# Optimization experiments

Measured on AMD Instinct MI355X. Metric: run time of the kernel, lower is better.

The kernel has to match this reference:

```python
import jax, jax.numpy as jnp
import numpy as np

B, S, D = 32, 256, 768
H = 12
HD = D // H           # 64
MLP = 4 * D           # 3072
EPS = 1e-5


def layernorm(x, g, b):
    mu = jnp.mean(x, axis=-1, keepdims=True)
    var = jnp.mean((x - mu) ** 2, axis=-1, keepdims=True)
    return (x - mu) * jax.lax.rsqrt(var + EPS) * g + b


def setup_inputs() -> dict:
    key = jax.random.key(0)
    ks = jax.random.split(key, 16)
    s_head = 1.0 / np.sqrt(HD)
    s_d = 1.0 / np.sqrt(D)
    s_mlp = 1.0 / np.sqrt(MLP)
    return {
        "x": jax.random.normal(ks[0], (B, S, D), dtype=jnp.float32),
        "g1": jnp.ones((D,), jnp.float32),
        "beta1": jnp.zeros((D,), jnp.float32),
        # per-head linear weights, torch Linear layout [out, in] stacked over heads
        "Wq": jax.random.uniform(ks[1], (H, HD, HD), jnp.float32, -s_head, s_head),
        "bq": jax.random.uniform(ks[2], (H, HD), jnp.float32, -s_head, s_head),
        "Wk": jax.random.uniform(ks[3], (H, HD, HD), jnp.float32, -s_head, s_head),
        "bk": jax.random.uniform(ks[4], (H, HD), jnp.float32, -s_head, s_head),
        "Wv": jax.random.uniform(ks[5], (H, HD, HD), jnp.float32, -s_head, s_head),
        "bv": jax.random.uniform(ks[6], (H, HD), jnp.float32, -s_head, s_head),
        "g2": jnp.ones((D,), jnp.float32),
        "beta2": jnp.zeros((D,), jnp.float32),
        "W1": jax.random.uniform(ks[7], (MLP, D), jnp.float32, -s_d, s_d),
        "bm1": jax.random.uniform(ks[8], (MLP,), jnp.float32, -s_d, s_d),
        "W2": jax.random.uniform(ks[9], (D, MLP), jnp.float32, -s_mlp, s_mlp),
        "bm2": jax.random.uniform(ks[10], (D,), jnp.float32, -s_mlp, s_mlp),
    }


def reference(x, g1, beta1, Wq, bq, Wk, bk, Wv, bv, g2, beta2, W1, bm1, W2, bm2):
    # --- MHA on norm1(x), fused over batch and heads ---
    h = layernorm(x, g1, beta1)                      # [B,S,D]
    hh = h.reshape(B, S, H, HD)                      # head split matches slicing in Mymha
    # q_e = sum_d hh_d * W[e,d]  (torch Linear: y = x @ W.T + b)
    q = jnp.einsum('bshd,hed->bshe', hh, Wq) + bq
    k = jnp.einsum('bshd,hed->bshe', hh, Wk) + bk
    v = jnp.einsum('bshd,hed->bshe', hh, Wv) + bv
    scores = jnp.einsum('bshe,bthe->bhst', q, k) / np.sqrt(HD)
    attn = jax.nn.softmax(scores, axis=-1)           # [B,H,S,S]
    ctx = jnp.einsum('bhst,bthe->bshe', attn, v).reshape(B, S, D)
    out = ctx + x
    # --- MLP on norm2(out) ---
    h2 = layernorm(out, g2, beta2)
    m = jax.nn.gelu(h2 @ W1.T + bm1, approximate=False)  # torch nn.GELU is exact erf
    out = m @ W2.T + bm2 + out
    return out
```

## Files before the change

kernel.cpp:

```cpp
#include <hip/hip_runtime.h>
#include <hip/hip_bf16.h>
#include <math.h>


static constexpr int Bn = 32, Sn = 256, Dn = 768, Hn = 12, HDn = 64, MLPn = 3072;
static constexpr int NT = Bn * Sn;

typedef unsigned short ushort_t;
typedef unsigned int u32;
typedef __attribute__((ext_vector_type(8))) short short8;
typedef __attribute__((ext_vector_type(4))) float f32x4;

__device__ __forceinline__ float bf2f(ushort_t u) { return __uint_as_float(((u32)u) << 16); }
__device__ __forceinline__ ushort_t f2bf(float f) {
  u32 u = __float_as_uint(f);
  u += 0x7fffu + ((u >> 16) & 1u);
  return (ushort_t)(u >> 16);
}

__device__ __forceinline__ void async_cp16(const ushort_t* g, ushort_t* l) {
  __builtin_amdgcn_global_load_lds(
      (const __attribute__((address_space(1))) u32*)g,
      (__attribute__((address_space(3))) u32*)l, 16, 0, 0);
}

__global__ __launch_bounds__(256) void k_prep(
    const float* __restrict__ Wq, const float* __restrict__ Wk,
    const float* __restrict__ Wv, const float* __restrict__ bq,
    const float* __restrict__ bk, const float* __restrict__ bv,
    const float* __restrict__ W1, const float* __restrict__ W2,
    const float* __restrict__ x, const float* __restrict__ g1,
    const float* __restrict__ be1,
    ushort_t* __restrict__ Wc, float* __restrict__ bc,
    ushort_t* __restrict__ W1b, ushort_t* __restrict__ W2b,
    ushort_t* __restrict__ hb)
{
  __shared__ float red[8];
  const int bx = blockIdx.x;
  const int tid = threadIdx.x;
  if (bx < 576) {
    int i = bx * 256 + tid;
    int h = i / 12288, rem = i - h * 12288;
    int mat = rem / 4096, w = rem - mat * 4096;
    const float* src = (mat == 0) ? Wq : ((mat == 1) ? Wk : Wv);
    Wc[i] = f2bf(src[h * 4096 + w]);
    if (i < Hn * 192) {
      int h2 = i / 192, r2 = i - h2 * 192;
      int m2 = r2 / 64, e2 = r2 - m2 * 64;
      const float* bs = (m2 == 0) ? bq : ((m2 == 1) ? bk : bv);
      bc[i] = bs[h2 * 64 + e2];
    }
  } else if (bx < 5184) {
    int j = bx - 576;
    const float* src = (j < 2304) ? W1 : W2;
    ushort_t* dst = (j < 2304) ? W1b : W2b;
    int i = (j % 2304) * 256 + tid;
    float4 v = ((const float4*)src)[i];
    ushort4 o;
    o.x = f2bf(v.x); o.y = f2bf(v.y); o.z = f2bf(v.z); o.w = f2bf(v.w);
    ((ushort4*)dst)[i] = o;
  } else {
    const int t = bx - 5184;
    float xv[3];
#pragma unroll
    for (int i = 0; i < 3; i++) xv[i] = x[(size_t)t * Dn + tid + i * 256];
    float s = xv[0] + xv[1] + xv[2];
#pragma unroll
    for (int off = 32; off > 0; off >>= 1) s += __shfl_down(s, off, 64);
    if ((tid & 63) == 0) red[tid >> 6] = s;
    __syncthreads();
    float mean = (red[0] + red[1] + red[2] + red[3]) * (1.0f / 768.0f);
    float d0 = xv[0] - mean, d1 = xv[1] - mean, d2 = xv[2] - mean;
    float s2 = d0 * d0 + d1 * d1 + d2 * d2;
#pragma unroll
    for (int off = 32; off > 0; off >>= 1) s2 += __shfl_down(s2, off, 64);
    if ((tid & 63) == 0) red[4 + (tid >> 6)] = s2;
    __syncthreads();
    float rstd = rsqrtf((red[4] + red[5] + red[6] + red[7]) * (1.0f / 768.0f) + 1e-5f);
#pragma unroll
    for (int i = 0; i < 3; i++) {
      int d = tid + i * 256;
      hb[(size_t)t * Dn + d] = f2bf((xv[i] - mean) * rstd * g1[d] + be1[d]);
    }
  }
}

__global__ __launch_bounds__(256) void k_qkv(
    const ushort_t* __restrict__ hb,
    const ushort_t* __restrict__ Wc,
    const float* __restrict__ bc,
    ushort_t* __restrict__ qo, ushort_t* __restrict__ ko, ushort_t* __restrict__ vt)
{
  __shared__ __align__(16) ushort_t As[128 * 72];
  __shared__ __align__(16) ushort_t Ws[192 * 72];
  const int blk = blockIdx.x;
  const int half = blk & 1;
  const int bh = blk >> 1;
  const int b_ = bh / Hn, h_ = bh - b_ * Hn;
  const int tid = threadIdx.x;
  const int t0 = b_ * Sn + half * 128;

  {
    int row = tid >> 1, seg = (tid & 1) * 32;
    const uint4* g = (const uint4*)(hb + (size_t)(t0 + row) * Dn + h_ * 64 + seg);
    uint4* s = (uint4*)(As + row * 72 + seg);
    s[0] = g[0]; s[1] = g[1]; s[2] = g[2]; s[3] = g[3];
  }
  {
    int rr = tid >> 2, seg = (tid & 3) * 16;
    const ushort_t* gw = Wc + h_ * 12288;
#pragma unroll
    for (int p = 0; p < 3; p++) {
      int R = p * 64 + rr;
      const uint4* g = (const uint4*)(gw + R * 64 + seg);
      uint4* s = (uint4*)(Ws + R * 72 + seg);
      s[0] = g[0]; s[1] = g[1];
    }
  }
  __syncthreads();

  const int wave = tid >> 6, lane = tid & 63;
  const int wm = (wave >> 1) * 64, wn = (wave & 1) * 96;
  const int lrow = lane & 15, quad = lane >> 4;

  f32x4 acc[4][6];
#pragma unroll
  for (int mi = 0; mi < 4; mi++)
#pragma unroll
    for (int ni = 0; ni < 6; ni++) acc[mi][ni] = (f32x4){0.f, 0.f, 0.f, 0.f};

#pragma unroll
  for (int kk = 0; kk < 2; kk++) {
    short8 af[4], wf[6];
#pragma unroll
    for (int mi = 0; mi < 4; mi++)
      af[mi] = *(const short8*)(As + (wm + mi * 16 + lrow) * 72 + kk * 32 + quad * 8);
#pragma unroll
    for (int ni = 0; ni < 6; ni++)
      wf[ni] = *(const short8*)(Ws + (wn + ni * 16 + lrow) * 72 + kk * 32 + quad * 8);
#pragma unroll
    for (int mi = 0; mi < 4; mi++)
#pragma unroll
      for (int ni = 0; ni < 6; ni++)
        acc[mi][ni] = __builtin_amdgcn_mfma_f32_16x16x32_bf16(af[mi], wf[ni], acc[mi][ni], 0, 0, 0);
  }

#pragma unroll
  for (int ni = 0; ni < 6; ni++) {
    int c = wn + ni * 16 + lrow;
    int mat = c >> 6, e = c & 63;
    float bb = bc[h_ * 192 + c];
    if (mat < 2) {
      ushort_t* dst = (mat == 0) ? qo : ko;
      size_t base = (((size_t)bh) * Sn + half * 128 + wm) * HDn + e;
#pragma unroll
      for (int mi = 0; mi < 4; mi++) {
#pragma unroll
        for (int r = 0; r < 4; r++) {
          int lr = mi * 16 + quad * 4 + r;
          dst[base + (size_t)lr * HDn] = f2bf(acc[mi][ni][r] + bb);
        }
      }
    } else {
      size_t rowb = ((size_t)bh * 64 + e) * Sn + half * 128 + wm + quad * 4;
#pragma unroll
      for (int mi = 0; mi < 4; mi++) {
        ushort4 pk;
        pk.x = f2bf(acc[mi][ni][0] + bb);
        pk.y = f2bf(acc[mi][ni][1] + bb);
        pk.z = f2bf(acc[mi][ni][2] + bb);
        pk.w = f2bf(acc[mi][ni][3] + bb);
        *(ushort4*)(vt + rowb + mi * 16) = pk;
      }
    }
  }
}

__global__ __launch_bounds__(256) void k_attn(
    const ushort_t* __restrict__ q,
    const ushort_t* __restrict__ kg_,
    const ushort_t* __restrict__ vt,
    const float* __restrict__ x,
    float* __restrict__ out1)
{
  __shared__ __align__(16) ushort_t Ks[64 * 72];
  __shared__ __align__(16) ushort_t Vts[64 * 264];
  __shared__ __align__(16) ushort_t Pw[4][16 * 72];
  const int blk = blockIdx.x;
  const int qtr = blk & 3, bh = blk >> 2;
  const int b_ = bh / Hn, h_ = bh - b_ * Hn;
  const int tid = threadIdx.x, wave = tid >> 6, lane = tid & 63;
  const int lr16 = lane & 15, quad = lane >> 4;
  const int s0 = qtr * 64 + wave * 16;

  {
    int r = tid >> 2, cseg = (tid & 3) * 64;
    const uint4* g = (const uint4*)(vt + ((size_t)bh * 64 + r) * Sn + cseg);
    uint4* s = (uint4*)(Vts + r * 264 + cseg);
#pragma unroll
    for (int i = 0; i < 8; i++) s[i] = g[i];
  }

  short8 qf[2];
  {
    const ushort_t* qg = q + ((size_t)bh * Sn + s0 + lr16) * HDn + quad * 8;
    qf[0] = *(const short8*)(qg);
    qf[1] = *(const short8*)(qg + 32);
  }

  f32x4 of[4];
#pragma unroll
  for (int et = 0; et < 4; et++) of[et] = (f32x4){0.f, 0.f, 0.f, 0.f};
  float mrow[4] = {-3.0e38f, -3.0e38f, -3.0e38f, -3.0e38f};
  float lsum[4] = {0.f, 0.f, 0.f, 0.f};

  const ushort_t* kgb = kg_ + (size_t)bh * Sn * HDn;

  for (int c = 0; c < 4; c++) {
    if (c) __syncthreads();
    {
      int row = tid >> 2, seg = (tid & 3) * 16;
      const uint4* g = (const uint4*)(kgb + (size_t)(c * 64 + row) * HDn + seg);
      uint4* s = (uint4*)(Ks + row * 72 + seg);
      s[0] = g[0]; s[1] = g[1];
    }
    __syncthreads();

    f32x4 sc[4];
#pragma unroll
    for (int ni = 0; ni < 4; ni++) sc[ni] = (f32x4){0.f, 0.f, 0.f, 0.f};
#pragma unroll
    for (int kk = 0; kk < 2; kk++) {
#pragma unroll
      for (int ni = 0; ni < 4; ni++) {
        short8 kf = *(const short8*)(Ks + (ni * 16 + lr16) * 72 + kk * 32 + quad * 8);
        sc[ni] = __builtin_amdgcn_mfma_f32_16x16x32_bf16(qf[kk], kf, sc[ni], 0, 0, 0);
      }
    }

    float alpha[4];
#pragma unroll
    for (int r = 0; r < 4; r++) {
      float m_ = fmaxf(fmaxf(sc[0][r], sc[1][r]), fmaxf(sc[2][r], sc[3][r]));
#pragma unroll
      for (int msk = 8; msk >= 1; msk >>= 1) m_ = fmaxf(m_, __shfl_xor(m_, msk, 64));
      float mn = fmaxf(mrow[r], m_);
      alpha[r] = __expf((mrow[r] - mn) * 0.125f);
      mrow[r] = mn;
    }
#pragma unroll
    for (int ni = 0; ni < 4; ni++) {
#pragma unroll
      for (int r = 0; r < 4; r++) {
        float p = __expf((sc[ni][r] - mrow[r]) * 0.125f);
        sc[ni][r] = p;
        Pw[wave][(quad * 4 + r) * 72 + ni * 16 + lr16] = f2bf(p);
      }
    }
#pragma unroll
    for (int r = 0; r < 4; r++) {
      float s_ = (sc[0][r] + sc[1][r]) + (sc[2][r] + sc[3][r]);
#pragma unroll
      for (int msk = 8; msk >= 1; msk >>= 1) s_ += __shfl_xor(s_, msk, 64);
      lsum[r] = lsum[r] * alpha[r] + s_;
    }
#pragma unroll
    for (int et = 0; et < 4; et++)
#pragma unroll
      for (int r = 0; r < 4; r++) of[et][r] *= alpha[r];

    short8 pf0 = *(const short8*)(&Pw[wave][lr16 * 72 + quad * 8]);
    short8 pf1 = *(const short8*)(&Pw[wave][lr16 * 72 + 32 + quad * 8]);
#pragma unroll
    for (int et = 0; et < 4; et++) {
      short8 vf0 = *(const short8*)(Vts + (et * 16 + lr16) * 264 + c * 64 + quad * 8);
      short8 vf1 = *(const short8*)(Vts + (et * 16 + lr16) * 264 + c * 64 + 32 + quad * 8);
      of[et] = __builtin_amdgcn_mfma_f32_16x16x32_bf16(pf0, vf0, of[et], 0, 0, 0);
      of[et] = __builtin_amdgcn_mfma_f32_16x16x32_bf16(pf1, vf1, of[et], 0, 0, 0);
    }
  }

  const size_t obase = ((size_t)b_ * Sn + s0) * Dn + h_ * 64;
#pragma unroll
  for (int r = 0; r < 4; r++) {
    float rl = 1.0f / lsum[r];
    int row = quad * 4 + r;
#pragma unroll
    for (int et = 0; et < 4; et++) {
      size_t idx = obase + (size_t)row * Dn + et * 16 + lr16;
      out1[idx] = of[et][r] * rl + x[idx];
    }
  }
}

__global__ __launch_bounds__(256) void k_ln2(
    const float* __restrict__ in, const float* __restrict__ g2,
    const float* __restrict__ be2, ushort_t* __restrict__ h2)
{
  const int t = blockIdx.x, tid = threadIdx.x;
  __shared__ float red[8];
  float xv[3];
#pragma unroll
  for (int i = 0; i < 3; i++) xv[i] = in[(size_t)t * Dn + tid + i * 256];
  float s = xv[0] + xv[1] + xv[2];
#pragma unroll
  for (int off = 32; off > 0; off >>= 1) s += __shfl_down(s, off, 64);
  if ((tid & 63) == 0) red[tid >> 6] = s;
  __syncthreads();
  float mean = (red[0] + red[1] + red[2] + red[3]) * (1.0f / 768.0f);
  float d0 = xv[0] - mean, d1 = xv[1] - mean, d2 = xv[2] - mean;
  float s2 = d0 * d0 + d1 * d1 + d2 * d2;
#pragma unroll
  for (int off = 32; off > 0; off >>= 1) s2 += __shfl_down(s2, off, 64);
  if ((tid & 63) == 0) red[4 + (tid >> 6)] = s2;
  __syncthreads();
  float rstd = rsqrtf((red[4] + red[5] + red[6] + red[7]) * (1.0f / 768.0f) + 1e-5f);
#pragma unroll
  for (int i = 0; i < 3; i++) {
    int d = tid + i * 256;
    h2[(size_t)t * Dn + d] = f2bf((xv[i] - mean) * rstd * g2[d] + be2[d]);
  }
}

__global__ __launch_bounds__(512, 2) void k_gemm1(
    const ushort_t* __restrict__ A,
    const ushort_t* __restrict__ Bw,
    const float* __restrict__ bias,
    ushort_t* __restrict__ CoutB)
{
  constexpr int KD = Dn;
  constexpr int NTILES = 12;
  constexpr int BUFU = 28672;
  __shared__ __align__(16) ushort_t smem[57344];
  const int b = blockIdx.x;
  const int xcd = b & 7, slot = b >> 3;
  const int cc = slot % 16, rloc = slot / 16;
  const int m0 = (xcd * 4 + rloc) * 256, n0 = cc * 192;
  const int tid = threadIdx.x;
  const int wave = tid >> 6, lane = tid & 63;
  const int wm2 = (wave >> 2) * 128, wn2 = (wave & 3) * 48;
  const int lrow = lane & 15, quad = lane >> 4;
  const int key = lrow & 7;

  f32x4 acc[8][3];
#pragma unroll
  for (int mi = 0; mi < 8; mi++)
#pragma unroll
    for (int ni = 0; ni < 3; ni++) acc[mi][ni] = (f32x4){0.f, 0.f, 0.f, 0.f};

  auto stageA = [&](int t, int half) {
    if (t >= NTILES) return;
    const int k0 = t * 64;
    ushort_t* tb = smem + (t & 1) * BUFU + half * 8192;
#pragma unroll
    for (int j = 0; j < 2; ++j) {
      int q = j * 512 + tid;
      int row = q >> 3;
      int sc = (q & 7) ^ (row & 7);
      async_cp16(A + (size_t)(m0 + half * 128 + row) * KD + k0 + sc * 8, tb + q * 8);
    }
  };
  auto stageB = [&](int t) {
    if (t >= NTILES) return;
    const int k0 = t * 64;
    ushort_t* tb = smem + (t & 1) * BUFU + 16384;
#pragma unroll
    for (int j = 0; j < 3; ++j) {
      int q = j * 512 + tid;
      int row = q >> 3;
      int sc = (q & 7) ^ (row & 7);
      async_cp16(Bw + (size_t)(n0 + row) * KD + k0 + sc * 8, tb + q * 8);
    }
  };

  stageA(0, 0); stageA(0, 1); stageB(0);
  asm volatile("s_waitcnt vmcnt(0)" ::: "memory");
  __builtin_amdgcn_s_barrier();
  __builtin_amdgcn_sched_barrier(0);

  short8 af[4][2], af2[4][2], bf0[3], bf1[3];
  for (int t = 0; t < NTILES; ++t) {
    const ushort_t* Ab = smem + (t & 1) * BUFU;
    const ushort_t* Bb = Ab + 16384;

#pragma unroll
    for (int mi = 0; mi < 4; ++mi)
#pragma unroll
      for (int kk = 0; kk < 2; ++kk)
        af[mi][kk] = *(const short8*)(Ab + (wm2 + mi * 16 + lrow) * 64 + (((kk << 2) + quad) ^ key) * 8);
#pragma unroll
    for (int ni = 0; ni < 3; ++ni)
      bf0[ni] = *(const short8*)(Bb + (wn2 + ni * 16 + lrow) * 64 + ((quad ^ key) * 8));
    stageA(t + 1, 0);
    __builtin_amdgcn_s_barrier();
    asm volatile("s_waitcnt lgkmcnt(0)" ::: "memory");
    __builtin_amdgcn_sched_barrier(0);
    __builtin_amdgcn_s_setprio(1);
#pragma unroll
    for (int mi = 0; mi < 4; ++mi)
#pragma unroll
      for (int ni = 0; ni < 3; ++ni)
        acc[mi][ni] = __builtin_amdgcn_mfma_f32_16x16x32_bf16(af[mi][0], bf0[ni], acc[mi][ni], 0, 0, 0);
    __builtin_amdgcn_s_setprio(0);
    __builtin_amdgcn_s_barrier();
    __builtin_amdgcn_sched_barrier(0);

#pragma unroll
    for (int ni = 0; ni < 3; ++ni)
      bf1[ni] = *(const short8*)(Bb + (wn2 + ni * 16 + lrow) * 64 + (((4 + quad) ^ key) * 8));
#pragma unroll
    for (int mi = 0; mi < 4; ++mi)
#pragma unroll
      for (int kk = 0; kk < 2; ++kk)
        af2[mi][kk] = *(const short8*)(Ab + (wm2 + 64 + mi * 16 + lrow) * 64 + (((kk << 2) + quad) ^ key) * 8);
    stageA(t + 1, 1);
    __builtin_amdgcn_s_barrier();
    asm volatile("s_waitcnt lgkmcnt(0)" ::: "memory");
    __builtin_amdgcn_sched_barrier(0);
    __builtin_amdgcn_s_setprio(1);
#pragma unroll
    for (int mi = 0; mi < 4; ++mi)
#pragma unroll
      for (int ni = 0; ni < 3; ++ni)
        acc[mi][ni] = __builtin_amdgcn_mfma_f32_16x16x32_bf16(af[mi][1], bf1[ni], acc[mi][ni], 0, 0, 0);
    __builtin_amdgcn_s_setprio(0);
    __builtin_amdgcn_s_barrier();
    __builtin_amdgcn_sched_barrier(0);

    stageB(t + 1);
    __builtin_amdgcn_s_barrier();
    __builtin_amdgcn_sched_barrier(0);
    __builtin_amdgcn_s_setprio(1);
#pragma unroll
    for (int mi = 0; mi < 4; ++mi)
#pragma unroll
      for (int ni = 0; ni < 3; ++ni)
        acc[4 + mi][ni] = __builtin_amdgcn_mfma_f32_16x16x32_bf16(af2[mi][0], bf0[ni], acc[4 + mi][ni], 0, 0, 0);
    __builtin_amdgcn_s_setprio(0);
    __builtin_amdgcn_s_barrier();
    __builtin_amdgcn_sched_barrier(0);

    __builtin_amdgcn_s_setprio(1);
#pragma unroll
    for (int mi = 0; mi < 4; ++mi)
#pragma unroll
      for (int ni = 0; ni < 3; ++ni)
        acc[4 + mi][ni] = __builtin_amdgcn_mfma_f32_16x16x32_bf16(af2[mi][1], bf1[ni], acc[4 + mi][ni], 0, 0, 0);
    __builtin_amdgcn_s_setprio(0);
    asm volatile("s_waitcnt vmcnt(0)" ::: "memory");
    __builtin_amdgcn_s_barrier();
    __builtin_amdgcn_sched_barrier(0);
  }

  float bwv[3];
#pragma unroll
  for (int ni = 0; ni < 3; ++ni) bwv[ni] = bias[n0 + wn2 + ni * 16 + lrow];
  __syncthreads();
#pragma unroll
  for (int mi = 0; mi < 8; ++mi) {
#pragma unroll
    for (int ni = 0; ni < 3; ++ni) {
      int col = wn2 + ni * 16 + lrow;
#pragma unroll
      for (int r = 0; r < 4; ++r) {
        int row = wm2 + mi * 16 + quad * 4 + r;
        float vv = acc[mi][ni][r] + bwv[ni];
        float u = vv * (0.7978845608f + 0.0356774081f * vv * vv);
        float o = vv / (1.0f + __expf(-2.0f * u));
        smem[row * 200 + col] = f2bf(o);
      }
    }
  }
  __syncthreads();
#pragma unroll
  for (int i = 0; i < 12; ++i) {
    int idx = i * 512 + tid;
    int rr = idx / 24, ck = idx - rr * 24;
    const uint4 v = *(const uint4*)(smem + rr * 200 + ck * 8);
    *(uint4*)(CoutB + (size_t)(m0 + rr) * MLPn + n0 + ck * 8) = v;
  }
}

__global__ __launch_bounds__(512, 2) void k_gemm2(
    const ushort_t* __restrict__ A,
    const ushort_t* __restrict__ Bw,
    const float* __restrict__ bias,
    const float* __restrict__ res,
    float* __restrict__ out)
{
  constexpr int KD = MLPn;
  constexpr int N = Dn;
  constexpr int NTILES = 48;
  constexpr int BUFU = 20480;
  __shared__ __align__(16) ushort_t smem[61440];
  const int b = blockIdx.x;
  const int xcd = b & 7, slot = b >> 3;
  const int cc = slot & 3, rloc = slot >> 2;
  const int m0 = (xcd * 8 + rloc) * 128, n0 = cc * 192;
  const int tid = threadIdx.x;
  const int wave = tid >> 6, lane = tid & 63;
  const int wm2 = (wave >> 2) * 64, wn2 = (wave & 3) * 48;
  const int lrow = lane & 15, quad = lane >> 4;
  const int key = lrow & 7;

  f32x4 acc[4][3];
#pragma unroll
  for (int mi = 0; mi < 4; mi++)
#pragma unroll
    for (int ni = 0; ni < 3; ni++) acc[mi][ni] = (f32x4){0.f, 0.f, 0.f, 0.f};

  auto stageT = [&](int t) {
    if (t >= NTILES) return;
    const int k0 = t * 64;
    ushort_t* bufA = smem + (t % 3) * BUFU;
    ushort_t* bufB = bufA + 8192;
#pragma unroll
    for (int j = 0; j < 2; ++j) {
      int q = j * 512 + tid;
      int row = q >> 3;
      int sc = (q & 7) ^ (row & 7);
      async_cp16(A + (size_t)(m0 + row) * KD + k0 + sc * 8, bufA + q * 8);
    }
#pragma unroll
    for (int j = 0; j < 3; ++j) {
      int q = j * 512 + tid;
      int row = q >> 3;
      int sc = (q & 7) ^ (row & 7);
      async_cp16(Bw + (size_t)(n0 + row) * KD + k0 + sc * 8, bufB + q * 8);
    }
  };

  stageT(0); stageT(1);
  asm volatile("s_waitcnt vmcnt(5)" ::: "memory");
  __builtin_amdgcn_s_barrier();
  __builtin_amdgcn_sched_barrier(0);

  short8 af[4], bf[3];
  for (int t = 0; t < NTILES; ++t) {
    const ushort_t* Ab = smem + (t % 3) * BUFU;
    const ushort_t* Bb = Ab + 8192;

#pragma unroll
    for (int mi = 0; mi < 4; ++mi)
      af[mi] = *(const short8*)(Ab + (wm2 + mi * 16 + lrow) * 64 + ((quad ^ key) * 8));
#pragma unroll
    for (int ni = 0; ni < 3; ++ni)
      bf[ni] = *(const short8*)(Bb + (wn2 + ni * 16 + lrow) * 64 + ((quad ^ key) * 8));
    stageT(t + 2);
    asm volatile("s_waitcnt lgkmcnt(0)" ::: "memory");
    __builtin_amdgcn_sched_barrier(0);
    __builtin_amdgcn_s_setprio(1);
#pragma unroll
    for (int mi = 0; mi < 4; ++mi)
#pragma unroll
      for (int ni = 0; ni < 3; ++ni)
        acc[mi][ni] = __builtin_amdgcn_mfma_f32_16x16x32_bf16(af[mi], bf[ni], acc[mi][ni], 0, 0, 0);
    __builtin_amdgcn_s_setprio(0);
#pragma unroll
    for (int mi = 0; mi < 4; ++mi)
      af[mi] = *(const short8*)(Ab + (wm2 + mi * 16 + lrow) * 64 + (((4 + quad) ^ key) * 8));
#pragma unroll
    for (int ni = 0; ni < 3; ++ni)
      bf[ni] = *(const short8*)(Bb + (wn2 + ni * 16 + lrow) * 64 + (((4 + quad) ^ key) * 8));
    asm volatile("s_waitcnt lgkmcnt(0)" ::: "memory");
    __builtin_amdgcn_sched_barrier(0);
    __builtin_amdgcn_s_setprio(1);
#pragma unroll
    for (int mi = 0; mi < 4; ++mi)
#pragma unroll
      for (int ni = 0; ni < 3; ++ni)
        acc[mi][ni] = __builtin_amdgcn_mfma_f32_16x16x32_bf16(af[mi], bf[ni], acc[mi][ni], 0, 0, 0);
    __builtin_amdgcn_s_setprio(0);
    if (t < NTILES - 2) {
      asm volatile("s_waitcnt vmcnt(5)" ::: "memory");
    } else {
      asm volatile("s_waitcnt vmcnt(0)" ::: "memory");
    }
    __builtin_amdgcn_s_barrier();
    __builtin_amdgcn_sched_barrier(0);
  }

#pragma unroll
  for (int ni = 0; ni < 3; ++ni) {
    int col = n0 + wn2 + ni * 16 + lrow;
    float bc = bias[col];
#pragma unroll
    for (int mi = 0; mi < 4; ++mi) {
#pragma unroll
      for (int r = 0; r < 4; ++r) {
        int row = m0 + wm2 + mi * 16 + quad * 4 + r;
        size_t idx = (size_t)row * N + col;
        out[idx] = acc[mi][ni][r] + bc + res[idx];
      }
    }
  }
}

extern "C" void kernel_launch(void* const* d_in, const int* in_sizes, int n_in,
                              void* d_out, int out_size, void* d_ws, size_t ws_size,
                              hipStream_t stream) {
  (void)in_sizes; (void)n_in; (void)out_size; (void)ws_size;
  const float* x   = (const float*)d_in[0];
  const float* g1  = (const float*)d_in[1];
  const float* be1 = (const float*)d_in[2];
  const float* Wq  = (const float*)d_in[3];
  const float* bq  = (const float*)d_in[4];
  const float* Wk  = (const float*)d_in[5];
  const float* bk  = (const float*)d_in[6];
  const float* Wv  = (const float*)d_in[7];
  const float* bv  = (const float*)d_in[8];
  const float* g2  = (const float*)d_in[9];
  const float* be2 = (const float*)d_in[10];
  const float* W1  = (const float*)d_in[11];
  const float* bm1 = (const float*)d_in[12];
  const float* W2  = (const float*)d_in[13];
  const float* bm2 = (const float*)d_in[14];
  float* outp = (float*)d_out;

  char* ws = (char*)d_ws;
  float*    out1 = (float*)ws;
  ushort_t* hb   = (ushort_t*)ws;
  ushort_t* qb   = (ushort_t*)(ws + 25165824);
  ushort_t* kb   = (ushort_t*)(ws + 37748736);
  ushort_t* vtb  = (ushort_t*)(ws + 50331648);
  ushort_t* h2   = qb;
  ushort_t* mb   = (ushort_t*)(ws + 37748736);
  ushort_t* Wc   = (ushort_t*)(ws + 88080384);
  ushort_t* W1b  = (ushort_t*)(ws + 88375296);
  ushort_t* W2b  = (ushort_t*)(ws + 93093888);
  float*    bcb  = (float*)(ws + 97812480);

  k_prep<<<dim3(5184 + NT), dim3(256), 0, stream>>>(Wq, Wk, Wv, bq, bk, bv, W1, W2,
                                                    x, g1, be1, Wc, bcb, W1b, W2b, hb);
  k_qkv<<<dim3(Bn * Hn * 2), dim3(256), 0, stream>>>(hb, Wc, bcb, qb, kb, vtb);
  k_attn<<<dim3(Bn * Hn * 4), dim3(256), 0, stream>>>(qb, kb, vtb, x, out1);
  k_ln2<<<dim3(NT), dim3(256), 0, stream>>>(out1, g2, be2, h2);
  k_gemm1<<<dim3(512), dim3(512), 0, stream>>>(h2, W1b, bm1, mb);
  k_gemm2<<<dim3(256), dim3(512), 0, stream>>>(mb, W2b, bm2, out1, outp);
}
```

Before: 270.9 us.

## Fuse QKV projection and attention into one kernel keeping Q/K/V in LDS

Merges the per-head QKV projection and the attention kernel so that each block computes Q, K and V for one (batch, head) into XOR-swizzled shared memory and then runs attention directly from LDS. This removes the global round-trip of Q, K and V^T and one kernel launch. The input loads now use async global-to-LDS copies, and softmax switches from online to a single pass over all 256 keys. The cost is 152 KB of LDS per block, which allows only one block per CU, and a grid of 384 blocks, down from 768 and 1536 before, which lowers occupancy and parallelism.

```diff
diff --git a/kernel.cpp b/kernel.cpp
--- a/kernel.cpp
+++ b/kernel.cpp
@@ -85,210 +85,171 @@
   }
 }
 
-__global__ __launch_bounds__(256) void k_qkv(
+__global__ __launch_bounds__(256) void k_fused(
     const ushort_t* __restrict__ hb,
     const ushort_t* __restrict__ Wc,
     const float* __restrict__ bc,
-    ushort_t* __restrict__ qo, ushort_t* __restrict__ ko, ushort_t* __restrict__ vt)
-{
-  __shared__ __align__(16) ushort_t As[128 * 72];
-  __shared__ __align__(16) ushort_t Ws[192 * 72];
-  const int blk = blockIdx.x;
-  const int half = blk & 1;
-  const int bh = blk >> 1;
-  const int b_ = bh / Hn, h_ = bh - b_ * Hn;
-  const int tid = threadIdx.x;
-  const int t0 = b_ * Sn + half * 128;
-
-  {
-    int row = tid >> 1, seg = (tid & 1) * 32;
-    const uint4* g = (const uint4*)(hb + (size_t)(t0 + row) * Dn + h_ * 64 + seg);
-    uint4* s = (uint4*)(As + row * 72 + seg);
-    s[0] = g[0]; s[1] = g[1]; s[2] = g[2]; s[3] = g[3];
-  }
-  {
-    int rr = tid >> 2, seg = (tid & 3) * 16;
-    const ushort_t* gw = Wc + h_ * 12288;
-#pragma unroll
-    for (int p = 0; p < 3; p++) {
-      int R = p * 64 + rr;
-      const uint4* g = (const uint4*)(gw + R * 64 + seg);
-      uint4* s = (uint4*)(Ws + R * 72 + seg);
-      s[0] = g[0]; s[1] = g[1];
-    }
-  }
-  __syncthreads();
-
-  const int wave = tid >> 6, lane = tid & 63;
-  const int wm = (wave >> 1) * 64, wn = (wave & 1) * 96;
-  const int lrow = lane & 15, quad = lane >> 4;
-
-  f32x4 acc[4][6];
-#pragma unroll
-  for (int mi = 0; mi < 4; mi++)
-#pragma unroll
-    for (int ni = 0; ni < 6; ni++) acc[mi][ni] = (f32x4){0.f, 0.f, 0.f, 0.f};
-
-#pragma unroll
-  for (int kk = 0; kk < 2; kk++) {
-    short8 af[4], wf[6];
-#pragma unroll
-    for (int mi = 0; mi < 4; mi++)
-      af[mi] = *(const short8*)(As + (wm + mi * 16 + lrow) * 72 + kk * 32 + quad * 8);
-#pragma unroll
-    for (int ni = 0; ni < 6; ni++)
-      wf[ni] = *(const short8*)(Ws + (wn + ni * 16 + lrow) * 72 + kk * 32 + quad * 8);
-#pragma unroll
-    for (int mi = 0; mi < 4; mi++)
-#pragma unroll
-      for (int ni = 0; ni < 6; ni++)
-        acc[mi][ni] = __builtin_amdgcn_mfma_f32_16x16x32_bf16(af[mi], wf[ni], acc[mi][ni], 0, 0, 0);
-  }
-
-#pragma unroll
-  for (int ni = 0; ni < 6; ni++) {
-    int c = wn + ni * 16 + lrow;
-    int mat = c >> 6, e = c & 63;
-    float bb = bc[h_ * 192 + c];
-    if (mat < 2) {
-      ushort_t* dst = (mat == 0) ? qo : ko;
-      size_t base = (((size_t)bh) * Sn + half * 128 + wm) * HDn + e;
-#pragma unroll
-      for (int mi = 0; mi < 4; mi++) {
-#pragma unroll
-        for (int r = 0; r < 4; r++) {
-          int lr = mi * 16 + quad * 4 + r;
-          dst[base + (size_t)lr * HDn] = f2bf(acc[mi][ni][r] + bb);
-        }
-      }
-    } else {
-      size_t rowb = ((size_t)bh * 64 + e) * Sn + half * 128 + wm + quad * 4;
-#pragma unroll
-      for (int mi = 0; mi < 4; mi++) {
-        ushort4 pk;
-        pk.x = f2bf(acc[mi][ni][0] + bb);
-        pk.y = f2bf(acc[mi][ni][1] + bb);
-        pk.z = f2bf(acc[mi][ni][2] + bb);
-        pk.w = f2bf(acc[mi][ni][3] + bb);
-        *(ushort4*)(vt + rowb + mi * 16) = pk;
-      }
-    }
-  }
-}
-
-__global__ __launch_bounds__(256) void k_attn(
-    const ushort_t* __restrict__ q,
-    const ushort_t* __restrict__ kg_,
-    const ushort_t* __restrict__ vt,
     const float* __restrict__ x,
     float* __restrict__ out1)
 {
-  __shared__ __align__(16) ushort_t Ks[64 * 72];
-  __shared__ __align__(16) ushort_t Vts[64 * 264];
-  __shared__ __align__(16) ushort_t Pw[4][16 * 72];
-  const int blk = blockIdx.x;
-  const int qtr = blk & 3, bh = blk >> 2;
+  __shared__ __align__(16) ushort_t smem[77824];
+  ushort_t* Qs  = smem;
+  ushort_t* Ks  = smem + 16384;
+  ushort_t* Vts = smem + 32768;
+  ushort_t* As  = smem + 49152;
+  ushort_t* Ws  = smem + 65536;
+  ushort_t* Pw  = smem + 49152;
+
+  const int bh = blockIdx.x;
   const int b_ = bh / Hn, h_ = bh - b_ * Hn;
-  const int tid = threadIdx.x, wave = tid >> 6, lane = tid & 63;
-  const int lr16 = lane & 15, quad = lane >> 4;
-  const int s0 = qtr * 64 + wave * 16;
+  const int tid = threadIdx.x;
+  const int wave = tid >> 6, lane = tid & 63;
+  const int lrow = lane & 15, quad = lane >> 4;
+  const int key = lrow & 7;
+  const int t0 = b_ * Sn;
 
   {
-    int r = tid >> 2, cseg = (tid & 3) * 64;
-    const uint4* g = (const uint4*)(vt + ((size_t)bh * 64 + r) * Sn + cseg);
-    uint4* s = (uint4*)(Vts + r * 264 + cseg);
-#pragma unroll
-    for (int i = 0; i < 8; i++) s[i] = g[i];
-  }
-
-  short8 qf[2];
-  {
-    const ushort_t* qg = q + ((size_t)bh * Sn + s0 + lr16) * HDn + quad * 8;
-    qf[0] = *(const short8*)(qg);
-    qf[1] = *(const short8*)(qg + 32);
-  }
-
-  f32x4 of[4];
-#pragma unroll
-  for (int et = 0; et < 4; et++) of[et] = (f32x4){0.f, 0.f, 0.f, 0.f};
-  float mrow[4] = {-3.0e38f, -3.0e38f, -3.0e38f, -3.0e38f};
-  float lsum[4] = {0.f, 0.f, 0.f, 0.f};
-
-  const ushort_t* kgb = kg_ + (size_t)bh * Sn * HDn;
-
-  for (int c = 0; c < 4; c++) {
-    if (c) __syncthreads();
-    {
-      int row = tid >> 2, seg = (tid & 3) * 16;
-      const uint4* g = (const uint4*)(kgb + (size_t)(c * 64 + row) * HDn + seg);
-      uint4* s = (uint4*)(Ks + row * 72 + seg);
-      s[0] = g[0]; s[1] = g[1];
-    }
-    __syncthreads();
-
-    f32x4 sc[4];
-#pragma unroll
-    for (int ni = 0; ni < 4; ni++) sc[ni] = (f32x4){0.f, 0.f, 0.f, 0.f};
+    const ushort_t* ga = hb + (size_t)t0 * Dn + h_ * 64;
+#pragma unroll
+    for (int j = 0; j < 8; ++j) {
+      int q = j * 256 + tid;
+      int row = q >> 3;
+      int sc = (q & 7) ^ (row & 7);
+      async_cp16(ga + (size_t)row * Dn + sc * 8, As + q * 8);
+    }
+    const ushort_t* gw = Wc + h_ * 12288;
+#pragma unroll
+    for (int j = 0; j < 6; ++j) {
+      int q = j * 256 + tid;
+      int row = q >> 3;
+      int sc = (q & 7) ^ (row & 7);
+      async_cp16(gw + row * 64 + sc * 8, Ws + q * 8);
+    }
+  }
+  asm volatile("s_waitcnt vmcnt(0)" ::: "memory");
+  __syncthreads();
+
+  const int wm = (wave >> 1) * 64, wn = (wave & 1) * 96;
+  for (int half = 0; half < 2; ++half) {
+    f32x4 acc[4][6];
+#pragma unroll
+    for (int mi = 0; mi < 4; mi++)
+#pragma unroll
+      for (int ni = 0; ni < 6; ni++) acc[mi][ni] = (f32x4){0.f, 0.f, 0.f, 0.f};
+
 #pragma unroll
     for (int kk = 0; kk < 2; kk++) {
-#pragma unroll
-      for (int ni = 0; ni < 4; ni++) {
-        short8 kf = *(const short8*)(Ks + (ni * 16 + lr16) * 72 + kk * 32 + quad * 8);
+      short8 af[4], wf[6];
+#pragma unroll
+      for (int mi = 0; mi < 4; mi++)
+        af[mi] = *(const short8*)(As + (half * 128 + wm + mi * 16 + lrow) * 64 + ((((kk << 2) + quad)) ^ key) * 8);
+#pragma unroll
+      for (int ni = 0; ni < 6; ni++)
+        wf[ni] = *(const short8*)(Ws + (wn + ni * 16 + lrow) * 64 + ((((kk << 2) + quad)) ^ key) * 8);
+#pragma unroll
+      for (int mi = 0; mi < 4; mi++)
+#pragma unroll
+        for (int ni = 0; ni < 6; ni++)
+          acc[mi][ni] = __builtin_amdgcn_mfma_f32_16x16x32_bf16(af[mi], wf[ni], acc[mi][ni], 0, 0, 0);
+    }
+
+#pragma unroll
+    for (int ni = 0; ni < 6; ni++) {
+      int c = wn + ni * 16 + lrow;
+      int mat = c >> 6, e = c & 63;
+      float bb = bc[h_ * 192 + c];
+      if (mat < 2) {
+        ushort_t* dst = (mat == 0) ? Qs : Ks;
+#pragma unroll
+        for (int mi = 0; mi < 4; mi++) {
+#pragma unroll
+          for (int r = 0; r < 4; r++) {
+            int srow = half * 128 + wm + mi * 16 + quad * 4 + r;
+            dst[srow * 64 + (((e >> 3) ^ (srow & 7)) << 3) + (e & 7)] = f2bf(acc[mi][ni][r] + bb);
+          }
+        }
+      } else {
+#pragma unroll
+        for (int mi = 0; mi < 4; mi++) {
+          int c4 = half * 128 + wm + mi * 16 + quad * 4;
+          ushort4 pk;
+          pk.x = f2bf(acc[mi][ni][0] + bb);
+          pk.y = f2bf(acc[mi][ni][1] + bb);
+          pk.z = f2bf(acc[mi][ni][2] + bb);
+          pk.w = f2bf(acc[mi][ni][3] + bb);
+          int cq = c4 >> 3;
+          *(ushort4*)(Vts + e * 256 + ((cq ^ (e & 7)) << 3) + (c4 & 7)) = pk;
+        }
+      }
+    }
+  }
+  __syncthreads();
+
+  ushort_t* Pme = Pw + wave * 4224;
+  for (int p = 0; p < 4; ++p) {
+    const int s0 = wave * 64 + p * 16;
+    short8 qf[2];
+#pragma unroll
+    for (int kk = 0; kk < 2; kk++)
+      qf[kk] = *(const short8*)(Qs + (s0 + lrow) * 64 + ((((kk << 2) + quad)) ^ key) * 8);
+
+    f32x4 sc[16];
+#pragma unroll
+    for (int ni = 0; ni < 16; ni++) sc[ni] = (f32x4){0.f, 0.f, 0.f, 0.f};
+#pragma unroll
+    for (int kk = 0; kk < 2; kk++) {
+#pragma unroll
+      for (int ni = 0; ni < 16; ni++) {
+        short8 kf = *(const short8*)(Ks + (ni * 16 + lrow) * 64 + ((((kk << 2) + quad)) ^ key) * 8);
         sc[ni] = __builtin_amdgcn_mfma_f32_16x16x32_bf16(qf[kk], kf, sc[ni], 0, 0, 0);
       }
     }
 
-    float alpha[4];
+    float inv[4];
 #pragma unroll
     for (int r = 0; r < 4; r++) {
-      float m_ = fmaxf(fmaxf(sc[0][r], sc[1][r]), fmaxf(sc[2][r], sc[3][r]));
+      float m_ = sc[0][r];
+#pragma unroll
+      for (int ni = 1; ni < 16; ni++) m_ = fmaxf(m_, sc[ni][r]);
 #pragma unroll
       for (int msk = 8; msk >= 1; msk >>= 1) m_ = fmaxf(m_, __shfl_xor(m_, msk, 64));
-      float mn = fmaxf(mrow[r], m_);
-      alpha[r] = __expf((mrow[r] - mn) * 0.125f);
-      mrow[r] = mn;
-    }
-#pragma unroll
-    for (int ni = 0; ni < 4; ni++) {
-#pragma unroll
-      for (int r = 0; r < 4; r++) {
-        float p = __expf((sc[ni][r] - mrow[r]) * 0.125f);
-        sc[ni][r] = p;
-        Pw[wave][(quad * 4 + r) * 72 + ni * 16 + lr16] = f2bf(p);
-      }
-    }
+      float s_ = 0.f;
+#pragma unroll
+      for (int ni = 0; ni < 16; ni++) {
+        float pv = __expf((sc[ni][r] - m_) * 0.125f);
+        s_ += pv;
+        Pme[(quad * 4 + r) * 264 + ni * 16 + lrow] = f2bf(pv);
+      }
+#pragma unroll
+      for (int msk = 8; msk >= 1; msk >>= 1) s_ += __shfl_xor(s_, msk, 64);
+      inv[r] = 1.0f / s_;
+    }
+    asm volatile("s_waitcnt lgkmcnt(0)" ::: "memory");
+    __builtin_amdgcn_sched_barrier(0);
+
+    f32x4 of[4];
+#pragma unroll
+    for (int et = 0; et < 4; et++) of[et] = (f32x4){0.f, 0.f, 0.f, 0.f};
+#pragma unroll
+    for (int ks = 0; ks < 8; ks++) {
+      short8 pf = *(const short8*)(Pme + lrow * 264 + ks * 32 + quad * 8);
+#pragma unroll
+      for (int et = 0; et < 4; et++) {
+        short8 vf = *(const short8*)(Vts + (et * 16 + lrow) * 256 + ((((ks << 2) + quad)) ^ key) * 8);
+        of[et] = __builtin_amdgcn_mfma_f32_16x16x32_bf16(pf, vf, of[et], 0, 0, 0);
+      }
+    }
+
+    const size_t obase = ((size_t)t0 + s0) * Dn + h_ * 64;
 #pragma unroll
     for (int r = 0; r < 4; r++) {
-      float s_ = (sc[0][r] + sc[1][r]) + (sc[2][r] + sc[3][r]);
-#pragma unroll
-      for (int msk = 8; msk >= 1; msk >>= 1) s_ += __shfl_xor(s_, msk, 64);
-      lsum[r] = lsum[r] * alpha[r] + s_;
-    }
-#pragma unroll
-    for (int et = 0; et < 4; et++)
-#pragma unroll
-      for (int r = 0; r < 4; r++) of[et][r] *= alpha[r];
-
-    short8 pf0 = *(const short8*)(&Pw[wave][lr16 * 72 + quad * 8]);
-    short8 pf1 = *(const short8*)(&Pw[wave][lr16 * 72 + 32 + quad * 8]);
-#pragma unroll
-    for (int et = 0; et < 4; et++) {
-      short8 vf0 = *(const short8*)(Vts + (et * 16 + lr16) * 264 + c * 64 + quad * 8);
-      short8 vf1 = *(const short8*)(Vts + (et * 16 + lr16) * 264 + c * 64 + 32 + quad * 8);
-      of[et] = __builtin_amdgcn_mfma_f32_16x16x32_bf16(pf0, vf0, of[et], 0, 0, 0);
-      of[et] = __builtin_amdgcn_mfma_f32_16x16x32_bf16(pf1, vf1, of[et], 0, 0, 0);
-    }
-  }
-
-  const size_t obase = ((size_t)b_ * Sn + s0) * Dn + h_ * 64;
-#pragma unroll
-  for (int r = 0; r < 4; r++) {
-    float rl = 1.0f / lsum[r];
-    int row = quad * 4 + r;
-#pragma unroll
-    for (int et = 0; et < 4; et++) {
-      size_t idx = obase + (size_t)row * Dn + et * 16 + lr16;
-      out1[idx] = of[et][r] * rl + x[idx];
+      float rl = inv[r];
+      int row = quad * 4 + r;
+#pragma unroll
+      for (int et = 0; et < 4; et++) {
+        size_t idx = obase + (size_t)row * Dn + et * 16 + lrow;
+        out1[idx] = of[et][r] * rl + x[idx];
+      }
     }
   }
 }
@@ -619,11 +580,8 @@
 
   char* ws = (char*)d_ws;
   float*    out1 = (float*)ws;
-  ushort_t* hb   = (ushort_t*)ws;
-  ushort_t* qb   = (ushort_t*)(ws + 25165824);
-  ushort_t* kb   = (ushort_t*)(ws + 37748736);
-  ushort_t* vtb  = (ushort_t*)(ws + 50331648);
-  ushort_t* h2   = qb;
+  ushort_t* hb   = (ushort_t*)(ws + 25165824);
+  ushort_t* h2   = (ushort_t*)(ws + 25165824);
   ushort_t* mb   = (ushort_t*)(ws + 37748736);
   ushort_t* Wc   = (ushort_t*)(ws + 88080384);
   ushort_t* W1b  = (ushort_t*)(ws + 88375296);
@@ -632,8 +590,7 @@
 
   k_prep<<<dim3(5184 + NT), dim3(256), 0, stream>>>(Wq, Wk, Wv, bq, bk, bv, W1, W2,
                                                     x, g1, be1, Wc, bcb, W1b, W2b, hb);
-  k_qkv<<<dim3(Bn * Hn * 2), dim3(256), 0, stream>>>(hb, Wc, bcb, qb, kb, vtb);
-  k_attn<<<dim3(Bn * Hn * 4), dim3(256), 0, stream>>>(qb, kb, vtb, x, out1);
+  k_fused<<<dim3(Bn * Hn), dim3(256), 0, stream>>>(hb, Wc, bcb, x, out1);
   k_ln2<<<dim3(NT), dim3(256), 0, stream>>>(out1, g2, be2, h2);
   k_gemm1<<<dim3(512), dim3(512), 0, stream>>>(h2, W1b, bm1, mb);
   k_gemm2<<<dim3(256), dim3(512), 0, stream>>>(mb, W2b, bm2, out1, outp);
```

Result: no change. 267.9 us (-1.1%).
